# Kernel tuning notes

Hardware: AMD Instinct MI355X
Metric: run time of the kernel (lower is better)

The kernel has to match this reference:

```python
import jax, jax.numpy as jnp
import numpy as np

N_NODES = 50000
N_EDGES = 800000
IN_CH = 64
HID = 128
EPS = 1e-12  # F.normalize default eps


def setup_inputs() -> dict:
    key = jax.random.key(0)
    ks = jax.random.split(key, 12)
    x = jax.random.normal(ks[0], (N_NODES, IN_CH), dtype=jnp.float32)
    edge_index = jax.random.randint(ks[1], (2, N_EDGES), 0, N_NODES, dtype=jnp.int64)
    def lin(k, out_c, in_c):
        bound = 1.0 / np.sqrt(in_c)
        return jax.random.uniform(k, (out_c, in_c), jnp.float32, -bound, bound)
    # layer 0: in->hid ; layers 1,2: hid->hid
    Wl0 = lin(ks[2], HID, IN_CH); bl0 = jnp.zeros((HID,), jnp.float32); Wr0 = lin(ks[3], HID, IN_CH)
    Wl1 = lin(ks[4], HID, HID);  bl1 = jnp.zeros((HID,), jnp.float32); Wr1 = lin(ks[5], HID, HID)
    Wl2 = lin(ks[6], HID, HID);  bl2 = jnp.zeros((HID,), jnp.float32); Wr2 = lin(ks[7], HID, HID)
    return {"x": x, "edge_index": edge_index,
            "Wl0": Wl0, "bl0": bl0, "Wr0": Wr0,
            "Wl1": Wl1, "bl1": bl1, "Wr1": Wr1,
            "Wl2": Wl2, "bl2": bl2, "Wr2": Wr2}


def _sage_conv(h, src, dst, Wl, bl, Wr, n_nodes):
    # mean aggregation of source-node features at target nodes
    msg = h[src]                                                   # [E, d]
    agg = jax.ops.segment_sum(msg, dst, num_segments=n_nodes)      # [N, d]
    cnt = jax.ops.segment_sum(jnp.ones((src.shape[0],), h.dtype), dst,
                              num_segments=n_nodes)                # [N]
    mean = agg / jnp.maximum(cnt, 1.0)[:, None]
    out = mean @ Wl.T + bl + h @ Wr.T                              # lin_l(agg)+lin_r(x)
    # L2 normalize (F.normalize, p=2)
    norm = jnp.maximum(jnp.linalg.norm(out, axis=-1, keepdims=True), EPS)
    return out / norm


def reference(x, edge_index, Wl0, bl0, Wr0, Wl1, bl1, Wr1, Wl2, bl2, Wr2):
    src, dst = edge_index[0], edge_index[1]
    n = x.shape[0]
    h = _sage_conv(x, src, dst, Wl0, bl0, Wr0, n)
    h = jax.nn.relu(h)  # dropout is identity in eval mode
    h = _sage_conv(h, src, dst, Wl1, bl1, Wr1, n)
    h = jax.nn.relu(h)
    h = _sage_conv(h, src, dst, Wl2, bl2, Wr2, n)
    return h
```

## Files before the change

### kernel.cpp

```cpp
#include <hip/hip_runtime.h>

#define NN 50000
#define NNP 50016
#define NE 800000
#define DIN 64
#define HD 128
#define NBUK 196
#define SB 196
#define BCAP 12288

typedef __attribute__((ext_vector_type(8))) short short8;
typedef __attribute__((ext_vector_type(4))) float f32x4;
typedef __attribute__((ext_vector_type(4))) unsigned short us4;
typedef __attribute__((ext_vector_type(8))) unsigned short us8;

__device__ __forceinline__ unsigned short f2bf(float f) {
    unsigned int u = __float_as_uint(f);
    u = (u + 0x7FFFu + ((u >> 16) & 1u)) >> 16;
    return (unsigned short)u;
}
__device__ __forceinline__ float bf2f(unsigned short u) {
    return __uint_as_float(((unsigned int)u) << 16);
}

#define LDS_SCAN256(a, t)                                 \
    for (int off_ = 1; off_ < 256; off_ <<= 1) {          \
        int add_ = ((t) >= off_) ? (a)[(t) - off_] : 0;   \
        __syncthreads();                                  \
        (a)[t] += add_;                                   \
        __syncthreads();                                  \
    }


__global__ __launch_bounds__(256) void bucket_count(const int* __restrict__ dst,
                                                    int* __restrict__ bcnt) {
    __shared__ int lc[256];
    int t = threadIdx.x;
    lc[t] = 0;
    __syncthreads();
    int base = blockIdx.x * 4096 + t * 16;
#pragma unroll
    for (int j = 0; j < 4; ++j) {
        int e = base + j * 4;
        if (e < NE) {
            int4 d = *(const int4*)(dst + e);
            atomicAdd(&lc[d.x >> 8], 1);
            atomicAdd(&lc[d.y >> 8], 1);
            atomicAdd(&lc[d.z >> 8], 1);
            atomicAdd(&lc[d.w >> 8], 1);
        }
    }
    __syncthreads();
    if (t < NBUK && lc[t] > 0) atomicAdd(&bcnt[t], lc[t]);
}

__global__ __launch_bounds__(256) void bucket_scan(const int* __restrict__ bcnt,
                                                   int* __restrict__ bbase,
                                                   int* __restrict__ rowptr) {
    __shared__ int sh[256];
    int t = threadIdx.x;
    int v = (t < NBUK) ? bcnt[t] : 0;
    sh[t] = v;
    __syncthreads();
    LDS_SCAN256(sh, t);
    if (t < NBUK) bbase[t] = sh[t] - v;
    if (t == NBUK - 1) bbase[NBUK] = sh[t];
    if (t == 0) rowptr[NN] = NE;
}

__global__ __launch_bounds__(256) void bucket_scatter(
    const int* __restrict__ src, const int* __restrict__ dst,
    const int* __restrict__ bbase, int* __restrict__ bfill,
    int* __restrict__ pairs) {
    __shared__ int cnt[256];
    __shared__ int incl[256];
    __shared__ int lfill[256];
    __shared__ int rung[256];
    __shared__ int buf[4096];
    __shared__ unsigned char bk[4096];
    int t = threadIdx.x;
    cnt[t] = 0;
    lfill[t] = 0;
    __syncthreads();
    int base = blockIdx.x * 4096 + t * 16;
#pragma unroll
    for (int j = 0; j < 4; ++j) {
        int e = base + j * 4;
        if (e < NE) {
            int4 d = *(const int4*)(dst + e);
            atomicAdd(&cnt[d.x >> 8], 1);
            atomicAdd(&cnt[d.y >> 8], 1);
            atomicAdd(&cnt[d.z >> 8], 1);
            atomicAdd(&cnt[d.w >> 8], 1);
        }
    }
    __syncthreads();
    incl[t] = cnt[t];
    __syncthreads();
    LDS_SCAN256(incl, t);
    int c = cnt[t];
    if (t < NBUK && c > 0) rung[t] = bbase[t] + atomicAdd(&bfill[t], c);
    __syncthreads();
#pragma unroll
    for (int j = 0; j < 4; ++j) {
        int e = base + j * 4;
        if (e < NE) {
            int4 s4 = *(const int4*)(src + e);
            int4 d4 = *(const int4*)(dst + e);
            int ss[4] = {s4.x, s4.y, s4.z, s4.w};
            int dd[4] = {d4.x, d4.y, d4.z, d4.w};
#pragma unroll
            for (int q = 0; q < 4; ++q) {
                int k = dd[q] >> 8;
                int p = (incl[k] - cnt[k]) + atomicAdd(&lfill[k], 1);
                buf[p] = ((dd[q] & 255) << 24) | ss[q];
                bk[p] = (unsigned char)k;
            }
        }
    }
    __syncthreads();
    int n = min(4096, NE - blockIdx.x * 4096);
    for (int i = t; i < n; i += 256) {
        int k = bk[i];
        pairs[rung[k] + (i - (incl[k] - cnt[k]))] = buf[i];
    }
}

__global__ __launch_bounds__(256) void build_csr(
    const int* __restrict__ pairs, const int* __restrict__ bbase,
    int* __restrict__ rowptr, float* __restrict__ invcnt,
    int* __restrict__ csr_src) {
    __shared__ int cnt[256];
    __shared__ int incl[256];
    __shared__ int lfill[256];
    __shared__ int sbuf[BCAP];
    int b = blockIdx.x, t = threadIdx.x;
    int pbeg = bbase[b], pend = bbase[b + 1];
    int sz = pend - pbeg;
    cnt[t] = 0;
    lfill[t] = 0;
    __syncthreads();
    for (int i = t; i < sz; i += 256)
        atomicAdd(&cnt[(unsigned)pairs[pbeg + i] >> 24], 1);
    __syncthreads();
    incl[t] = cnt[t];
    __syncthreads();
    LDS_SCAN256(incl, t);
    int node = b * 256 + t;
    int c = cnt[t];
    if (node < NN) {
        rowptr[node] = pbeg + incl[t] - c;
        invcnt[node] = 1.0f / (float)(c > 0 ? c : 1);
    }
    if (sz <= BCAP) {
        for (int i = t; i < sz; i += 256) {
            int pr = pairs[pbeg + i];
            int ld = (unsigned)pr >> 24;
            sbuf[(incl[ld] - cnt[ld]) + atomicAdd(&lfill[ld], 1)] = pr & 0xFFFFFF;
        }
        __syncthreads();
        for (int i = t; i < sz; i += 256) csr_src[pbeg + i] = sbuf[i];
    } else {
        for (int i = t; i < sz; i += 256) {
            int pr = pairs[pbeg + i];
            int ld = (unsigned)pr >> 24;
            csr_src[pbeg + (incl[ld] - cnt[ld]) + atomicAdd(&lfill[ld], 1)] = pr & 0xFFFFFF;
        }
    }
}


__device__ __forceinline__ void pack_one(const float* Wl, const float* Wr, int D,
                                         unsigned short* Wpk, int i) {
    int j = i & 7;
    int lane = (i >> 3) & 63;
    int ct = (i >> 9) & 7;
    int ks = i >> 12;
    int k = ks * 32 + ((lane >> 4) << 3) + j;
    int c = ct * 16 + (lane & 15);
    float v = (k < D) ? Wl[c * D + k] : Wr[c * D + (k - D)];
    Wpk[i] = f2bf(v);
}

#define PACK_BLOCKS 320
#define CONV_BLOCKS 3125

__global__ __launch_bounds__(256) void prep(
    const float* __restrict__ Wl0, const float* __restrict__ Wr0,
    const float* __restrict__ Wl1, const float* __restrict__ Wr1,
    const float* __restrict__ Wl2, const float* __restrict__ Wr2,
    unsigned short* __restrict__ Wpk0, unsigned short* __restrict__ Wpk1,
    unsigned short* __restrict__ Wpk2,
    const float* __restrict__ x, unsigned short* __restrict__ A0,
    int* __restrict__ meta) {
    const int S0 = 2 * DIN * HD;
    const int S12 = 2 * HD * HD;
    int b = blockIdx.x;
    int t = threadIdx.x;
    if (b < PACK_BLOCKS) {
        int i = b * 256 + t;
        if (i < S0) { pack_one(Wl0, Wr0, DIN, Wpk0, i); return; }
        int j = i - S0;
        if (j < S12) { pack_one(Wl1, Wr1, HD, Wpk1, j); return; }
        int m = j - S12;
        if (m < S12) pack_one(Wl2, Wr2, HD, Wpk2, m);
        return;
    }
    if (b < PACK_BLOCKS + CONV_BLOCKS) {
        int i = (b - PACK_BLOCKS) * 256 + t;
        int row = i >> 4, c4 = i & 15;
        float4 v = ((const float4*)(x + (size_t)row * DIN))[c4];
        us4 o = {f2bf(v.x), f2bf(v.y), f2bf(v.z), f2bf(v.w)};
        *(us4*)(A0 + (size_t)row * 128 + 64 + c4 * 4) = o;
        return;
    }
    meta[t] = 0;
    meta[t + 256] = 0;
}


__global__ __launch_bounds__(256) void gather_mean_x(
    const int* __restrict__ rowptr, const int* __restrict__ csr_src,
    const float* __restrict__ invcnt, unsigned short* __restrict__ A0) {
    int tid = threadIdx.x;
    int n = blockIdx.x * 8 + (tid >> 5);
    int c8 = tid & 7;
    int eg = (tid >> 3) & 3;
    int beg = rowptr[n], end = rowptr[n + 1];
    float acc[8] = {};
    const unsigned short* hb = A0 + 64 + (size_t)c8 * 8;
    int e = beg + eg;
    for (; e + 12 < end; e += 16) {
        int i0 = csr_src[e], i1 = csr_src[e + 4], i2 = csr_src[e + 8], i3 = csr_src[e + 12];
        us8 v0 = *(const us8*)(hb + (size_t)i0 * 128);
        us8 v1 = *(const us8*)(hb + (size_t)i1 * 128);
        us8 v2 = *(const us8*)(hb + (size_t)i2 * 128);
        us8 v3 = *(const us8*)(hb + (size_t)i3 * 128);
#pragma unroll
        for (int j = 0; j < 8; ++j)
            acc[j] += (bf2f(v0[j]) + bf2f(v1[j])) + (bf2f(v2[j]) + bf2f(v3[j]));
    }
    for (; e < end; e += 4) {
        us8 v0 = *(const us8*)(hb + (size_t)csr_src[e] * 128);
#pragma unroll
        for (int j = 0; j < 8; ++j) acc[j] += bf2f(v0[j]);
    }
#pragma unroll
    for (int j = 0; j < 8; ++j) {
        acc[j] += __shfl_xor(acc[j], 8, 64);
        acc[j] += __shfl_xor(acc[j], 16, 64);
    }
    if (eg == 0) {
        float ic = invcnt[n];
        us8 o;
#pragma unroll
        for (int j = 0; j < 8; ++j) o[j] = f2bf(acc[j] * ic);
        *(us8*)(A0 + (size_t)n * 128 + c8 * 8) = o;
    }
}


__global__ __launch_bounds__(256) void gather_mean_h(
    const unsigned short* __restrict__ A12, const int* __restrict__ rowptr,
    const int* __restrict__ csr_src, const float* __restrict__ invcnt,
    unsigned short* __restrict__ Am) {
    int tid = threadIdx.x;
    int n = blockIdx.x * 4 + (tid >> 6);
    int lane = tid & 63;
    int c8 = lane & 15;
    int eg = lane >> 4;
    int beg = rowptr[n], end = rowptr[n + 1];
    float acc[8] = {};
    const unsigned short* hb = A12 + 128 + (size_t)c8 * 8;
    int e = beg + eg;
    for (; e + 12 < end; e += 16) {
        int i0 = csr_src[e], i1 = csr_src[e + 4], i2 = csr_src[e + 8], i3 = csr_src[e + 12];
        us8 v0 = *(const us8*)(hb + (size_t)i0 * 256);
        us8 v1 = *(const us8*)(hb + (size_t)i1 * 256);
        us8 v2 = *(const us8*)(hb + (size_t)i2 * 256);
        us8 v3 = *(const us8*)(hb + (size_t)i3 * 256);
#pragma unroll
        for (int j = 0; j < 8; ++j)
            acc[j] += (bf2f(v0[j]) + bf2f(v1[j])) + (bf2f(v2[j]) + bf2f(v3[j]));
    }
    for (; e < end; e += 4) {
        us8 v0 = *(const us8*)(hb + (size_t)csr_src[e] * 256);
#pragma unroll
        for (int j = 0; j < 8; ++j) acc[j] += bf2f(v0[j]);
    }
#pragma unroll
    for (int j = 0; j < 8; ++j) {
        acc[j] += __shfl_xor(acc[j], 16, 64);
        acc[j] += __shfl_xor(acc[j], 32, 64);
    }
    if (eg == 0) {
        float ic = invcnt[n];
        us8 o;
#pragma unroll
        for (int j = 0; j < 8; ++j) o[j] = f2bf(acc[j] * ic);
        *(us8*)(Am + (size_t)n * 256 + c8 * 8) = o;
    }
}


template <int K, bool RELU, bool F32OUT, bool BF16H>
__global__ __launch_bounds__(256) void linear_mfma(
    const unsigned short* __restrict__ A, const unsigned short* __restrict__ Wpk,
    const float* __restrict__ bias, float* __restrict__ outF,
    unsigned short* __restrict__ Hn ) {
    constexpr int NK = K / 32;
    __shared__ float rsum[2][32];
    int tid = threadIdx.x;
    int lane = tid & 63, w = tid >> 6;
    int rg = w >> 1, cg = w & 1;
    int r0 = blockIdx.x * 32 + rg * 16;
    int row_l = lane & 15, kb = lane >> 4;

    const unsigned short* Arow = A + (size_t)(r0 + row_l) * K + kb * 8;
    const unsigned short* Wp = Wpk + ((size_t)(cg * 4) * 64 + lane) * 8;

    f32x4 acc[4] = {{0.f, 0.f, 0.f, 0.f}, {0.f, 0.f, 0.f, 0.f},
                    {0.f, 0.f, 0.f, 0.f}, {0.f, 0.f, 0.f, 0.f}};
#pragma unroll
    for (int ks = 0; ks < NK; ++ks) {
        short8 a = *(const short8*)(Arow + ks * 32);
#pragma unroll
        for (int t = 0; t < 4; ++t) {
            short8 b = *(const short8*)(Wp + ((size_t)ks * 8 + t) * 64 * 8);
            acc[t] = __builtin_amdgcn_mfma_f32_16x16x32_bf16(a, b, acc[t], 0, 0, 0);
        }
    }

    float sq[4] = {0.f, 0.f, 0.f, 0.f};
#pragma unroll
    for (int t = 0; t < 4; ++t) {
        float bv = bias[cg * 64 + t * 16 + row_l];
#pragma unroll
        for (int r = 0; r < 4; ++r) {
            acc[t][r] += bv;
            sq[r] = fmaf(acc[t][r], acc[t][r], sq[r]);
        }
    }
#pragma unroll
    for (int off = 1; off < 16; off <<= 1)
#pragma unroll
        for (int r = 0; r < 4; ++r) sq[r] += __shfl_xor(sq[r], off, 64);

    if (row_l == 0) {
#pragma unroll
        for (int r = 0; r < 4; ++r) rsum[cg][rg * 16 + kb * 4 + r] = sq[r];
    }
    __syncthreads();

    int rbase = rg * 16 + kb * 4;
#pragma unroll
    for (int r = 0; r < 4; ++r) {
        int row = r0 + kb * 4 + r;
        if (row >= NN) continue;
        float n2 = rsum[0][rbase + r] + rsum[1][rbase + r];
        float inv = 1.0f / fmaxf(sqrtf(n2), 1e-12f);
#pragma unroll
        for (int t = 0; t < 4; ++t) {
            float v = acc[t][r] * inv;
            if (RELU) v = fmaxf(v, 0.f);
            int c = cg * 64 + t * 16 + row_l;
            if (F32OUT) outF[(size_t)row * HD + c] = v;
            if (BF16H) Hn[(size_t)row * 256 + c] = f2bf(v);
        }
    }
}


static inline size_t align256(size_t x) { return (x + 255) & ~(size_t)255; }

extern "C" void kernel_launch(void* const* d_in, const int* in_sizes, int n_in,
                              void* d_out, int out_size, void* d_ws, size_t ws_size,
                              hipStream_t stream) {
    const float* x   = (const float*)d_in[0];
    const int*   ei  = (const int*)d_in[1];
    const float* Wl0 = (const float*)d_in[2];
    const float* bl0 = (const float*)d_in[3];
    const float* Wr0 = (const float*)d_in[4];
    const float* Wl1 = (const float*)d_in[5];
    const float* bl1 = (const float*)d_in[6];
    const float* Wr1 = (const float*)d_in[7];
    const float* Wl2 = (const float*)d_in[8];
    const float* bl2 = (const float*)d_in[9];
    const float* Wr2 = (const float*)d_in[10];

    const int* src = ei;
    const int* dst = ei + NE;

    char* p = (char*)d_ws;
    size_t off = 0;
    int* meta = (int*)(p + off);            off = align256(off + 512 * 4);
    int* bbase = (int*)(p + off);           off = align256(off + 256 * 4);
    int* rowptr = (int*)(p + off);          off = align256(off + (size_t)(NN + 1) * 4);
    int* csr_src = (int*)(p + off);         off = align256(off + (size_t)NE * 4);
    float* invcnt = (float*)(p + off);      off = align256(off + (size_t)NN * 4);
    int* pairs = (int*)(p + off);           off = align256(off + (size_t)NE * 4);
    unsigned short* A0 = (unsigned short*)(p + off);   off = align256(off + (size_t)NNP * 128 * 2);
    unsigned short* A12 = (unsigned short*)(p + off);  off = align256(off + (size_t)NNP * 256 * 2);
    unsigned short* Wpk0 = (unsigned short*)(p + off); off = align256(off + (size_t)2 * DIN * HD * 2);
    unsigned short* Wpk1 = (unsigned short*)(p + off); off = align256(off + (size_t)2 * HD * HD * 2);
    unsigned short* Wpk2 = (unsigned short*)(p + off); off = align256(off + (size_t)2 * HD * HD * 2);
    (void)ws_size; (void)n_in; (void)in_sizes; (void)out_size;

    int* bcnt = meta;
    int* bfill = meta + 256;
    float* out = (float*)d_out;

    prep<<<PACK_BLOCKS + CONV_BLOCKS + 1, 256, 0, stream>>>(
        Wl0, Wr0, Wl1, Wr1, Wl2, Wr2, Wpk0, Wpk1, Wpk2, x, A0, meta);

    bucket_count<<<SB, 256, 0, stream>>>(dst, bcnt);
    bucket_scan<<<1, 256, 0, stream>>>(bcnt, bbase, rowptr);
    bucket_scatter<<<SB, 256, 0, stream>>>(src, dst, bbase, bfill, pairs);
    build_csr<<<NBUK, 256, 0, stream>>>(pairs, bbase, rowptr, invcnt, csr_src);

    const int LG = NNP / 32;
    const int GX = NN / 8;
    const int GH = NN / 4;

    gather_mean_x<<<GX, 256, 0, stream>>>(rowptr, csr_src, invcnt, A0);
    linear_mfma<2 * DIN, true, false, true><<<LG, 256, 0, stream>>>(
        A0, Wpk0, bl0, nullptr, A12 + 128);

    gather_mean_h<<<GH, 256, 0, stream>>>(A12, rowptr, csr_src, invcnt, A12);
    linear_mfma<2 * HD, true, false, true><<<LG, 256, 0, stream>>>(
        A12, Wpk1, bl1, nullptr, A12 + 128);

    gather_mean_h<<<GH, 256, 0, stream>>>(A12, rowptr, csr_src, invcnt, A12);
    linear_mfma<2 * HD, false, true, false><<<LG, 256, 0, stream>>>(
        A12, Wpk2, bl2, out, nullptr);
}
```

Measured before the change: 166.8 us.

## Fuse neighbor mean gather with MFMA linear layer via swizzled LDS tile

Merges each layer's gather-mean kernel and MFMA linear kernel into one sage_layer kernel. The mean rows for a 32-node tile are built in a XOR-swizzled LDS buffer and fed straight into the MFMA, while the self features are read from global memory. This removes the round trip of the mean matrix through global memory and three kernel launches, and splits features into separate ping-pong H buffers. In exchange the gather runs with far fewer blocks (32 nodes per block, 8 per wave serially), which lowers the parallelism available to hide latency on the irregular gather.

New measurement: 197.5 us. 18.4% more time.

```diff
diff --git a/kernel.cpp b/kernel.cpp
--- a/kernel.cpp
+++ b/kernel.cpp
@@ -191,7 +191,7 @@
     const float* __restrict__ Wl2, const float* __restrict__ Wr2,
     unsigned short* __restrict__ Wpk0, unsigned short* __restrict__ Wpk1,
     unsigned short* __restrict__ Wpk2,
-    const float* __restrict__ x, unsigned short* __restrict__ A0,
+    const float* __restrict__ x, unsigned short* __restrict__ Xbf,
     int* __restrict__ meta) {
     const int S0 = 2 * DIN * HD;
     const int S12 = 2 * HD * HD;
@@ -211,7 +211,7 @@
         int row = i >> 4, c4 = i & 15;
         float4 v = ((const float4*)(x + (size_t)row * DIN))[c4];
         us4 o = {f2bf(v.x), f2bf(v.y), f2bf(v.z), f2bf(v.w)};
-        *(us4*)(A0 + (size_t)row * 128 + 64 + c4 * 4) = o;
+        *(us4*)(Xbf + (size_t)row * DIN + c4 * 4) = o;
         return;
     }
     meta[t] = 0;
@@ -219,111 +219,127 @@
 }
 
 
-__global__ __launch_bounds__(256) void gather_mean_x(
-    const int* __restrict__ rowptr, const int* __restrict__ csr_src,
-    const float* __restrict__ invcnt, unsigned short* __restrict__ A0) {
-    int tid = threadIdx.x;
-    int n = blockIdx.x * 8 + (tid >> 5);
-    int c8 = tid & 7;
-    int eg = (tid >> 3) & 3;
-    int beg = rowptr[n], end = rowptr[n + 1];
-    float acc[8] = {};
-    const unsigned short* hb = A0 + 64 + (size_t)c8 * 8;
-    int e = beg + eg;
-    for (; e + 12 < end; e += 16) {
-        int i0 = csr_src[e], i1 = csr_src[e + 4], i2 = csr_src[e + 8], i3 = csr_src[e + 12];
-        us8 v0 = *(const us8*)(hb + (size_t)i0 * 128);
-        us8 v1 = *(const us8*)(hb + (size_t)i1 * 128);
-        us8 v2 = *(const us8*)(hb + (size_t)i2 * 128);
-        us8 v3 = *(const us8*)(hb + (size_t)i3 * 128);
-#pragma unroll
-        for (int j = 0; j < 8; ++j)
-            acc[j] += (bf2f(v0[j]) + bf2f(v1[j])) + (bf2f(v2[j]) + bf2f(v3[j]));
-    }
-    for (; e < end; e += 4) {
-        us8 v0 = *(const us8*)(hb + (size_t)csr_src[e] * 128);
-#pragma unroll
-        for (int j = 0; j < 8; ++j) acc[j] += bf2f(v0[j]);
-    }
-#pragma unroll
-    for (int j = 0; j < 8; ++j) {
-        acc[j] += __shfl_xor(acc[j], 8, 64);
-        acc[j] += __shfl_xor(acc[j], 16, 64);
-    }
-    if (eg == 0) {
-        float ic = invcnt[n];
-        us8 o;
-#pragma unroll
-        for (int j = 0; j < 8; ++j) o[j] = f2bf(acc[j] * ic);
-        *(us8*)(A0 + (size_t)n * 128 + c8 * 8) = o;
-    }
-}
-
-
-__global__ __launch_bounds__(256) void gather_mean_h(
-    const unsigned short* __restrict__ A12, const int* __restrict__ rowptr,
+template <int D, bool RELU, bool F32OUT>
+__global__ __launch_bounds__(256) void sage_layer(
+    const unsigned short* __restrict__ Hin, const int* __restrict__ rowptr,
     const int* __restrict__ csr_src, const float* __restrict__ invcnt,
-    unsigned short* __restrict__ Am) {
-    int tid = threadIdx.x;
-    int n = blockIdx.x * 4 + (tid >> 6);
-    int lane = tid & 63;
-    int c8 = lane & 15;
-    int eg = lane >> 4;
-    int beg = rowptr[n], end = rowptr[n + 1];
-    float acc[8] = {};
-    const unsigned short* hb = A12 + 128 + (size_t)c8 * 8;
-    int e = beg + eg;
-    for (; e + 12 < end; e += 16) {
-        int i0 = csr_src[e], i1 = csr_src[e + 4], i2 = csr_src[e + 8], i3 = csr_src[e + 12];
-        us8 v0 = *(const us8*)(hb + (size_t)i0 * 256);
-        us8 v1 = *(const us8*)(hb + (size_t)i1 * 256);
-        us8 v2 = *(const us8*)(hb + (size_t)i2 * 256);
-        us8 v3 = *(const us8*)(hb + (size_t)i3 * 256);
-#pragma unroll
-        for (int j = 0; j < 8; ++j)
-            acc[j] += (bf2f(v0[j]) + bf2f(v1[j])) + (bf2f(v2[j]) + bf2f(v3[j]));
-    }
-    for (; e < end; e += 4) {
-        us8 v0 = *(const us8*)(hb + (size_t)csr_src[e] * 256);
-#pragma unroll
-        for (int j = 0; j < 8; ++j) acc[j] += bf2f(v0[j]);
-    }
-#pragma unroll
-    for (int j = 0; j < 8; ++j) {
-        acc[j] += __shfl_xor(acc[j], 16, 64);
-        acc[j] += __shfl_xor(acc[j], 32, 64);
-    }
-    if (eg == 0) {
-        float ic = invcnt[n];
-        us8 o;
-#pragma unroll
-        for (int j = 0; j < 8; ++j) o[j] = f2bf(acc[j] * ic);
-        *(us8*)(Am + (size_t)n * 256 + c8 * 8) = o;
-    }
-}
-
-
-template <int K, bool RELU, bool F32OUT, bool BF16H>
-__global__ __launch_bounds__(256) void linear_mfma(
-    const unsigned short* __restrict__ A, const unsigned short* __restrict__ Wpk,
-    const float* __restrict__ bias, float* __restrict__ outF,
-    unsigned short* __restrict__ Hn ) {
+    const unsigned short* __restrict__ Wpk, const float* __restrict__ bias,
+    float* __restrict__ outF, unsigned short* __restrict__ Hout) {
+    constexpr int K = 2 * D;
     constexpr int NK = K / 32;
+    constexpr int NKH = NK / 2;
+    constexpr int NCH = D / 8;
+    __shared__ unsigned short mean_lds[32 * D];
     __shared__ float rsum[2][32];
+
     int tid = threadIdx.x;
     int lane = tid & 63, w = tid >> 6;
+    int n0 = blockIdx.x * 32;
+
+    if (D == 128) {
+        int c8 = lane & 15, eg = lane >> 4;
+        const unsigned short* hb = Hin + (size_t)c8 * 8;
+#pragma unroll
+        for (int i = 0; i < 8; ++i) {
+            int nl = w * 8 + i;
+            int n = n0 + nl;
+            float acc[8] = {};
+            if (n < NN) {
+                int beg = rowptr[n], end = rowptr[n + 1];
+                int e = beg + eg;
+                for (; e + 12 < end; e += 16) {
+                    int i0 = csr_src[e], i1 = csr_src[e + 4];
+                    int i2 = csr_src[e + 8], i3 = csr_src[e + 12];
+                    us8 v0 = *(const us8*)(hb + (size_t)i0 * D);
+                    us8 v1 = *(const us8*)(hb + (size_t)i1 * D);
+                    us8 v2 = *(const us8*)(hb + (size_t)i2 * D);
+                    us8 v3 = *(const us8*)(hb + (size_t)i3 * D);
+#pragma unroll
+                    for (int j = 0; j < 8; ++j)
+                        acc[j] += (bf2f(v0[j]) + bf2f(v1[j])) + (bf2f(v2[j]) + bf2f(v3[j]));
+                }
+                for (; e < end; e += 4) {
+                    us8 v0 = *(const us8*)(hb + (size_t)csr_src[e] * D);
+#pragma unroll
+                    for (int j = 0; j < 8; ++j) acc[j] += bf2f(v0[j]);
+                }
+#pragma unroll
+                for (int j = 0; j < 8; ++j) {
+                    acc[j] += __shfl_xor(acc[j], 16, 64);
+                    acc[j] += __shfl_xor(acc[j], 32, 64);
+                }
+            }
+            if (eg == 0) {
+                float ic = (n < NN) ? invcnt[n] : 0.f;
+                us8 o;
+#pragma unroll
+                for (int j = 0; j < 8; ++j) o[j] = f2bf(acc[j] * ic);
+                *(us8*)&mean_lds[(nl * NCH + (c8 ^ (nl & 7))) * 8] = o;
+            }
+        }
+    } else {
+        int c8 = lane & 7, eg = (lane >> 3) & 3, half = lane >> 5;
+        const unsigned short* hb = Hin + (size_t)c8 * 8;
+#pragma unroll
+        for (int i = 0; i < 4; ++i) {
+            int nl = w * 8 + i * 2 + half;
+            int n = n0 + nl;
+            float acc[8] = {};
+            if (n < NN) {
+                int beg = rowptr[n], end = rowptr[n + 1];
+                int e = beg + eg;
+                for (; e + 12 < end; e += 16) {
+                    int i0 = csr_src[e], i1 = csr_src[e + 4];
+                    int i2 = csr_src[e + 8], i3 = csr_src[e + 12];
+                    us8 v0 = *(const us8*)(hb + (size_t)i0 * D);
+                    us8 v1 = *(const us8*)(hb + (size_t)i1 * D);
+                    us8 v2 = *(const us8*)(hb + (size_t)i2 * D);
+                    us8 v3 = *(const us8*)(hb + (size_t)i3 * D);
+#pragma unroll
+                    for (int j = 0; j < 8; ++j)
+                        acc[j] += (bf2f(v0[j]) + bf2f(v1[j])) + (bf2f(v2[j]) + bf2f(v3[j]));
+                }
+                for (; e < end; e += 4) {
+                    us8 v0 = *(const us8*)(hb + (size_t)csr_src[e] * D);
+#pragma unroll
+                    for (int j = 0; j < 8; ++j) acc[j] += bf2f(v0[j]);
+                }
+#pragma unroll
+                for (int j = 0; j < 8; ++j) {
+                    acc[j] += __shfl_xor(acc[j], 8, 64);
+                    acc[j] += __shfl_xor(acc[j], 16, 64);
+                }
+            }
+            if (eg == 0) {
+                float ic = (n < NN) ? invcnt[n] : 0.f;
+                us8 o;
+#pragma unroll
+                for (int j = 0; j < 8; ++j) o[j] = f2bf(acc[j] * ic);
+                *(us8*)&mean_lds[(nl * NCH + (c8 ^ (nl & 7))) * 8] = o;
+            }
+        }
+    }
+    __syncthreads();
+
     int rg = w >> 1, cg = w & 1;
-    int r0 = blockIdx.x * 32 + rg * 16;
+    int r0 = n0 + rg * 16;
     int row_l = lane & 15, kb = lane >> 4;
-
-    const unsigned short* Arow = A + (size_t)(r0 + row_l) * K + kb * 8;
+    int lrow = rg * 16 + row_l;
+
+    const unsigned short* Hrow = Hin + (size_t)(r0 + row_l) * D + kb * 8;
     const unsigned short* Wp = Wpk + ((size_t)(cg * 4) * 64 + lane) * 8;
 
     f32x4 acc[4] = {{0.f, 0.f, 0.f, 0.f}, {0.f, 0.f, 0.f, 0.f},
                     {0.f, 0.f, 0.f, 0.f}, {0.f, 0.f, 0.f, 0.f}};
 #pragma unroll
     for (int ks = 0; ks < NK; ++ks) {
-        short8 a = *(const short8*)(Arow + ks * 32);
+        short8 a;
+        if (ks < NKH) {
+            int chunk = ks * 4 + kb;
+            a = *(const short8*)&mean_lds[(lrow * NCH + (chunk ^ (lrow & 7))) * 8];
+        } else {
+            a = *(const short8*)(Hrow + (ks - NKH) * 32);
+        }
 #pragma unroll
         for (int t = 0; t < 4; ++t) {
             short8 b = *(const short8*)(Wp + ((size_t)ks * 8 + t) * 64 * 8);
@@ -365,7 +381,7 @@
             if (RELU) v = fmaxf(v, 0.f);
             int c = cg * 64 + t * 16 + row_l;
             if (F32OUT) outF[(size_t)row * HD + c] = v;
-            if (BF16H) Hn[(size_t)row * 256 + c] = f2bf(v);
+            else Hout[(size_t)row * HD + c] = f2bf(v);
         }
     }
 }
@@ -399,8 +415,9 @@
     int* csr_src = (int*)(p + off);         off = align256(off + (size_t)NE * 4);
     float* invcnt = (float*)(p + off);      off = align256(off + (size_t)NN * 4);
     int* pairs = (int*)(p + off);           off = align256(off + (size_t)NE * 4);
-    unsigned short* A0 = (unsigned short*)(p + off);   off = align256(off + (size_t)NNP * 128 * 2);
-    unsigned short* A12 = (unsigned short*)(p + off);  off = align256(off + (size_t)NNP * 256 * 2);
+    unsigned short* Xbf = (unsigned short*)(p + off);  off = align256(off + (size_t)NNP * DIN * 2);
+    unsigned short* H0 = (unsigned short*)(p + off);   off = align256(off + (size_t)NNP * HD * 2);
+    unsigned short* H1 = (unsigned short*)(p + off);   off = align256(off + (size_t)NNP * HD * 2);
     unsigned short* Wpk0 = (unsigned short*)(p + off); off = align256(off + (size_t)2 * DIN * HD * 2);
     unsigned short* Wpk1 = (unsigned short*)(p + off); off = align256(off + (size_t)2 * HD * HD * 2);
     unsigned short* Wpk2 = (unsigned short*)(p + off); off = align256(off + (size_t)2 * HD * HD * 2);
@@ -411,7 +428,7 @@
     float* out = (float*)d_out;
 
     prep<<<PACK_BLOCKS + CONV_BLOCKS + 1, 256, 0, stream>>>(
-        Wl0, Wr0, Wl1, Wr1, Wl2, Wr2, Wpk0, Wpk1, Wpk2, x, A0, meta);
+        Wl0, Wr0, Wl1, Wr1, Wl2, Wr2, Wpk0, Wpk1, Wpk2, x, Xbf, meta);
 
     bucket_count<<<SB, 256, 0, stream>>>(dst, bcnt);
     bucket_scan<<<1, 256, 0, stream>>>(bcnt, bbase, rowptr);
@@ -419,18 +436,11 @@
     build_csr<<<NBUK, 256, 0, stream>>>(pairs, bbase, rowptr, invcnt, csr_src);
 
     const int LG = NNP / 32;
-    const int GX = NN / 8;
-    const int GH = NN / 4;
-
-    gather_mean_x<<<GX, 256, 0, stream>>>(rowptr, csr_src, invcnt, A0);
-    linear_mfma<2 * DIN, true, false, true><<<LG, 256, 0, stream>>>(
-        A0, Wpk0, bl0, nullptr, A12 + 128);
-
-    gather_mean_h<<<GH, 256, 0, stream>>>(A12, rowptr, csr_src, invcnt, A12);
-    linear_mfma<2 * HD, true, false, true><<<LG, 256, 0, stream>>>(
-        A12, Wpk1, bl1, nullptr, A12 + 128);
-
-    gather_mean_h<<<GH, 256, 0, stream>>>(A12, rowptr, csr_src, invcnt, A12);
-    linear_mfma<2 * HD, false, true, false><<<LG, 256, 0, stream>>>(
-        A12, Wpk2, bl2, out, nullptr);
-}
+
+    sage_layer<DIN, true, false><<<LG, 256, 0, stream>>>(
+        Xbf, rowptr, csr_src, invcnt, Wpk0, bl0, nullptr, H0);
+    sage_layer<HD, true, false><<<LG, 256, 0, stream>>>(
+        H0, rowptr, csr_src, invcnt, Wpk1, bl1, nullptr, H1);
+    sage_layer<HD, false, true><<<LG, 256, 0, stream>>>(
+        H1, rowptr, csr_src, invcnt, Wpk2, bl2, out, nullptr);
+}
```
